# Kernel tuning notes

Measured on AMD Instinct MI355X. Metric: run time of the kernel, lower is better.

Reference implementation:

```python
import jax, jax.numpy as jnp
import numpy as np

D = 512            # d_model
H = 4              # num_heads
DK = D // 2        # total key dim (expand_k = 0.5)
DV = D             # total value dim (expand_v = 1.0)
HK = DK // H       # per-head key dim  = 64
HV = DV // H       # per-head value dim = 128
GATE_LOW_RANK = 16
GATE_LOGIT_NORMALIZER = 16.0
LN_EPS = 1e-5


def setup_inputs() -> dict:
    key = jax.random.key(0)
    ks = jax.random.split(key, 9)
    B, S = 2, 16384
    g = lambda k, shape, scale: (jax.random.normal(k, shape, dtype=jnp.float32) * scale)
    return {
        "x":    g(ks[0], (B, S, D), 1.0),
        "Wq":   g(ks[1], (D, DK), D ** -0.5),
        "Wk":   g(ks[2], (D, DK), D ** -0.5),
        "Wv":   g(ks[3], (D, DV), D ** -0.5),
        "Wg":   g(ks[4], (D, DV), D ** -0.5),
        "Wgk1": g(ks[5], (D, GATE_LOW_RANK), D ** -0.5),
        "Wgk2": g(ks[6], (GATE_LOW_RANK, DK), GATE_LOW_RANK ** -0.5),
        "bgk2": jnp.zeros((DK,), jnp.float32),
        "Wo":   g(ks[7], (DV, D), DV ** -0.5),
    }


def _gla(x, Wq, Wk, Wv, Wg, Wgk1, Wgk2, bgk2, Wo):
    B, S, _ = x.shape
    q = (x @ Wq).reshape(B, S, H, HK) * (HK ** -0.5)   # [B,S,H,HK]
    k = (x @ Wk).reshape(B, S, H, HK)
    v = (x @ Wv).reshape(B, S, H, HV)
    g = (x @ Wg).reshape(B, S, H, HV)                  # output gate
    # low-rank forget gate, in log space
    gk = jax.nn.log_sigmoid((x @ Wgk1) @ Wgk2 + bgk2) / GATE_LOGIT_NORMALIZER
    gk = gk.reshape(B, S, H, HK)

    # gated linear recurrence over time:
    #   h_t = diag(exp(gk_t)) h_{t-1} + k_t^T v_t ;  o_t = q_t h_t
    def step(h, inp):
        q_t, k_t, v_t, gk_t = inp                      # [B,H,HK] / [B,H,HV]
        h = jnp.exp(gk_t)[..., None] * h + k_t[..., None] * v_t[..., None, :]
        o_t = jnp.einsum('bhk,bhkv->bhv', q_t, h)
        return h, o_t

    h0 = jnp.zeros((B, H, HK, HV), x.dtype)
    xs = (q.swapaxes(0, 1), k.swapaxes(0, 1), v.swapaxes(0, 1), gk.swapaxes(0, 1))
    _, o = jax.lax.scan(step, h0, xs)                  # o: [S,B,H,HV]
    o = o.swapaxes(0, 1)                               # [B,S,H,HV]

    # per-head LayerNorm (no affine) + swish output gate
    mu = o.mean(-1, keepdims=True)
    var = ((o - mu) ** 2).mean(-1, keepdims=True)
    o = (o - mu) * jax.lax.rsqrt(var + LN_EPS)
    o = o * jax.nn.silu(g)
    return o.reshape(B, S, DV) @ Wo                    # [B,S,D]


def reference(x, Wq, Wk, Wv, Wg, Wgk1, Wgk2, bgk2, Wo):
    return _gla(x, Wq, Wk, Wv, Wg, Wgk1, Wgk2, bgk2, Wo)
```

## Files before the change

kernel.cpp:

```cpp
#include <hip/hip_runtime.h>
#include <hip/hip_bf16.h>


typedef __hip_bfloat16 bf16;
typedef _Float16 f16;
typedef _Float16 half8 __attribute__((ext_vector_type(8)));
typedef float f32x4 __attribute__((ext_vector_type(4)));
typedef short short8 __attribute__((ext_vector_type(8)));

#define DEV static __device__ __forceinline__

DEV float b2f(bf16 v) { return __bfloat162float(v); }
DEV bf16 f2b(float v) { return __float2bfloat16(v); }
DEV float bits2f(unsigned int u16) {
    union { unsigned int u; float f; } c; c.u = u16 << 16; return c.f;
}
DEV short f2bs(float v) {
    union { bf16 h; short s; } u; u.h = __float2bfloat16(v); return u.s;
}
DEV unsigned short f2bu(float v) {
    union { bf16 h; unsigned short s; } u; u.h = __float2bfloat16(v); return u.s;
}
DEV short f2hs(float v) {
    union { f16 h; short s; } u; u.h = (f16)v; return u.s;
}
DEV float fast_rcp(float v) { return __builtin_amdgcn_rcpf(v); }

DEV float ldf(const float* p) { return *p; }
DEV float ldf(const bf16* p) { return b2f(*p); }
DEV void stf(float* p, float v) { *p = v; }
DEV void stf(bf16* p, float v) { *p = f2b(v); }

DEV float4 ld4(const float* p) { return *(const float4*)p; }
DEV float4 ld4(const bf16* p) {
    const uint2 r = *(const uint2*)p;
    return make_float4(bits2f(r.x & 0xffffu), bits2f(r.x >> 16),
                       bits2f(r.y & 0xffffu), bits2f(r.y >> 16));
}

DEV half8 ld8h(const float* p) {
    const float4 a = *(const float4*)p, b = *(const float4*)(p + 4);
    half8 h;
    h[0] = (f16)a.x; h[1] = (f16)a.y; h[2] = (f16)a.z; h[3] = (f16)a.w;
    h[4] = (f16)b.x; h[5] = (f16)b.y; h[6] = (f16)b.z; h[7] = (f16)b.w;
    return h;
}
DEV half8 ld8h(const f16* p) { return *(const half8*)p; }

DEV f32x4 mfma_bf(short8 a, short8 b, f32x4 c) {
    return __builtin_amdgcn_mfma_f32_16x16x32_bf16(a, b, c, 0, 0, 0);
}
DEV f32x4 mfma_h(half8 a, half8 b, f32x4 c) {
    return __builtin_amdgcn_mfma_f32_16x16x32_f16(a, b, c, 0, 0, 0);
}

DEV void gl_lds16(const f16* g, f16* l) {
    __builtin_amdgcn_global_load_lds(
        (const __attribute__((address_space(1))) void*)g,
        (__attribute__((address_space(3))) void*)l, 16, 0, 0);
}

DEV size_t voff(int v, int t) {
    return (size_t)(((((v >> 4) * 2 + (t >> 5)) * 4 + ((t >> 3) & 3)) * 16
                     + (v & 15)) * 8 + (t & 7));
}

__global__ __launch_bounds__(256) void cvt_xh_k(
    const float* __restrict__ x, f16* __restrict__ xh)
{
    const size_t i = ((size_t)blockIdx.x * 256 + threadIdx.x) * 8;
    *(half8*)&xh[i] = ld8h(&x[i]);
}

__global__ __launch_bounds__(256) void cvt_wt_k(
    const float* __restrict__ Wq, const float* __restrict__ Wk,
    const float* __restrict__ Wv, const float* __restrict__ Wg,
    const float* __restrict__ Wo, f16* __restrict__ Wt)
{
    __shared__ float tile[64][65];
    const int nb = blockIdx.x * 64;
    const int tid = threadIdx.x;
    const float* src; int nloc, N;
    if (nb < 256)       { src = Wq; N = 256; nloc = nb; }
    else if (nb < 512)  { src = Wk; N = 256; nloc = nb - 256; }
    else if (nb < 1024) { src = Wv; N = 512; nloc = nb - 512; }
    else if (nb < 1536) { src = Wg; N = 512; nloc = nb - 1024; }
    else                { src = Wo; N = 512; nloc = nb - 1536; }
    for (int k0 = 0; k0 < 512; k0 += 64) {
        for (int e = tid; e < 4096; e += 256) {
            const int i = e >> 6, j = e & 63;
            tile[i][j] = src[(size_t)(k0 + i) * N + nloc + j];
        }
        __syncthreads();
        for (int e = tid; e < 4096; e += 256) {
            const int j = e >> 6, i = e & 63;
            Wt[(size_t)(nb + j) * 512 + k0 + i] = (f16)tile[i][j];
        }
        __syncthreads();
    }
}

__global__ __launch_bounds__(256) void proj_gemm_k(
    const f16* __restrict__ A, const f16* __restrict__ Wt,
    bf16* __restrict__ Qb, bf16* __restrict__ Kb,
    bf16* __restrict__ VF, bf16* __restrict__ GOb)
{
    __shared__ __align__(16) f16 As[128][64];
    __shared__ __align__(16) f16 Bs[128][64];
    const int bm = blockIdx.x * 128;
    const int bn = blockIdx.y * 128;
    const int tid = threadIdx.x;
    const int lane = tid & 63;
    const int wid = tid >> 6;
    const int wr = wid >> 1, wc = wid & 1;
    const int al = lane & 15;
    const int kg = lane >> 4;
    const int al7 = al & 7;

    f32x4 acc[4][4];
#pragma unroll
    for (int m = 0; m < 4; ++m)
#pragma unroll
        for (int n = 0; n < 4; ++n)
#pragma unroll
            for (int r = 0; r < 4; ++r) acc[m][n][r] = 0.f;

    const int srow = wid * 32 + (lane >> 3);
    const int sswz = ((lane & 7) ^ (lane >> 3)) << 3;
    const f16* ap = A + (size_t)(bm + srow) * 512 + sswz;
    const f16* bp = Wt + (size_t)(bn + srow) * 512 + sswz;

    for (int k0 = 0; k0 < 512; k0 += 64) {
        if (k0) __syncthreads();
#pragma unroll
        for (int i = 0; i < 4; ++i) {
            gl_lds16(ap + (size_t)i * 8 * 512 + k0, &As[wid * 32 + i * 8][0]);
            gl_lds16(bp + (size_t)i * 8 * 512 + k0, &Bs[wid * 32 + i * 8][0]);
        }
        __syncthreads();
#pragma unroll
        for (int ks = 0; ks < 2; ++ks) {
            half8 af[4], bfr[4];
            const int sp = ((ks * 4 + kg) ^ al7) << 3;
#pragma unroll
            for (int m = 0; m < 4; ++m)
                af[m] = *(const half8*)&As[wr * 64 + m * 16 + al][sp];
#pragma unroll
            for (int n = 0; n < 4; ++n)
                bfr[n] = *(const half8*)&Bs[wc * 64 + n * 16 + al][sp];
#pragma unroll
            for (int m = 0; m < 4; ++m)
#pragma unroll
                for (int n = 0; n < 4; ++n)
                    acc[m][n] = mfma_h(af[m], bfr[n], acc[m][n]);
        }
    }

    const int r00 = bm + wr * 64 + kg * 4;
    const int c00 = bn + wc * 64 + al;
    const int seg = bn >> 8;
    if (seg == 0) {
#pragma unroll
        for (int m = 0; m < 4; ++m)
#pragma unroll
            for (int n = 0; n < 4; ++n)
#pragma unroll
                for (int r = 0; r < 4; ++r)
                    stf(&Qb[(size_t)(r00 + m * 16 + r) * 256 + c00 + n * 16],
                        acc[m][n][r] * 0.125f);
    } else if (seg == 1) {
#pragma unroll
        for (int m = 0; m < 4; ++m)
#pragma unroll
            for (int n = 0; n < 4; ++n)
#pragma unroll
                for (int r = 0; r < 4; ++r)
                    stf(&Kb[(size_t)(r00 + m * 16 + r) * 256 + (c00 - 256) + n * 16],
                        acc[m][n][r]);
    } else if (seg <= 3) {
#pragma unroll
        for (int m = 0; m < 4; ++m) {
            const int row0 = r00 + m * 16;
            const int bi = row0 >> 14;
            const int chunk = (row0 >> 6) & 255;
            const int tc = row0 & 63;
#pragma unroll
            for (int n = 0; n < 4; ++n) {
                const int col = c00 - 512 + n * 16;
                const int h = col >> 7, v = col & 127;
                bf16* dst = VF + (size_t)((bi * 4 + h) * 256 + chunk) * 8192
                               + voff(v, tc);
                ushort4 pk;
                pk.x = f2bu(acc[m][n][0]); pk.y = f2bu(acc[m][n][1]);
                pk.z = f2bu(acc[m][n][2]); pk.w = f2bu(acc[m][n][3]);
                *(ushort4*)dst = pk;
            }
        }
    } else {
#pragma unroll
        for (int m = 0; m < 4; ++m)
#pragma unroll
            for (int n = 0; n < 4; ++n)
#pragma unroll
                for (int r = 0; r < 4; ++r) {
                    const float v = acc[m][n][r];
                    const float sil = v * fast_rcp(1.f + __expf(-v));
                    stf(&GOb[(size_t)(r00 + m * 16 + r) * 512 + (c00 - 1024) + n * 16],
                        sil);
                }
    }
}

__global__ __launch_bounds__(256) void gemm_bt_k(
    const f16* __restrict__ A, const f16* __restrict__ Bt,
    float* __restrict__ C)
{
    __shared__ __align__(16) f16 As[128][64];
    __shared__ __align__(16) f16 Bs[128][64];
    const int bm = blockIdx.x * 128;
    const int bn = blockIdx.y * 128;
    const int tid = threadIdx.x;
    const int lane = tid & 63;
    const int wid = tid >> 6;
    const int wr = wid >> 1, wc = wid & 1;
    const int al = lane & 15;
    const int kg = lane >> 4;
    const int al7 = al & 7;

    f32x4 acc[4][4];
#pragma unroll
    for (int m = 0; m < 4; ++m)
#pragma unroll
        for (int n = 0; n < 4; ++n)
#pragma unroll
            for (int r = 0; r < 4; ++r) acc[m][n][r] = 0.f;

    const int srow = wid * 32 + (lane >> 3);
    const int sswz = ((lane & 7) ^ (lane >> 3)) << 3;
    const f16* ap = A + (size_t)(bm + srow) * 512 + sswz;
    const f16* bp = Bt + (size_t)(bn + srow) * 512 + sswz;

    for (int k0 = 0; k0 < 512; k0 += 64) {
        if (k0) __syncthreads();
#pragma unroll
        for (int i = 0; i < 4; ++i) {
            gl_lds16(ap + (size_t)i * 8 * 512 + k0, &As[wid * 32 + i * 8][0]);
            gl_lds16(bp + (size_t)i * 8 * 512 + k0, &Bs[wid * 32 + i * 8][0]);
        }
        __syncthreads();
#pragma unroll
        for (int ks = 0; ks < 2; ++ks) {
            half8 af[4], bfr[4];
            const int sp = ((ks * 4 + kg) ^ al7) << 3;
#pragma unroll
            for (int m = 0; m < 4; ++m)
                af[m] = *(const half8*)&As[wr * 64 + m * 16 + al][sp];
#pragma unroll
            for (int n = 0; n < 4; ++n)
                bfr[n] = *(const half8*)&Bs[wc * 64 + n * 16 + al][sp];
#pragma unroll
            for (int m = 0; m < 4; ++m)
#pragma unroll
                for (int n = 0; n < 4; ++n)
                    acc[m][n] = mfma_h(af[m], bfr[n], acc[m][n]);
        }
    }
    const int r0 = bm + wr * 64 + kg * 4;
    const int c0 = bn + wc * 64 + al;
#pragma unroll
    for (int m = 0; m < 4; ++m)
#pragma unroll
        for (int n = 0; n < 4; ++n)
#pragma unroll
            for (int r = 0; r < 4; ++r)
                C[(size_t)(r0 + m * 16 + r) * 512 + c0 + n * 16] = acc[m][n][r];
}

template <typename GKT>
__global__ __launch_bounds__(256) void gate_mfma_k(
    const f16* __restrict__ xh, const float* __restrict__ Wgk1,
    const float* __restrict__ Wgk2, const float* __restrict__ bgk2,
    GKT* __restrict__ GK)
{
    __shared__ __align__(16) f16 As[128][40];
    __shared__ __align__(16) f16 w1s[16][520];
    __shared__ float tls[128][17];
    const int bm = blockIdx.x * 128;
    const int tid = threadIdx.x;
    const int lane = tid & 63;
    const int wid = tid >> 6;
    const int al = lane & 15;
    const int kg = lane >> 4;
    const int kg8 = kg * 8;

    for (int e = tid; e < 8192; e += 256) {
        const int kk = e >> 4, n = e & 15;
        w1s[n][kk] = (f16)Wgk1[e];
    }

    f32x4 acc[2];
#pragma unroll
    for (int m = 0; m < 2; ++m)
#pragma unroll
        for (int r = 0; r < 4; ++r) acc[m][r] = 0.f;

    const int ar = tid >> 1;
    const int ac = (tid & 1) * 16;
    for (int k0 = 0; k0 < 512; k0 += 32) {
        {
            const f16* ap = xh + (size_t)(bm + ar) * 512 + k0 + ac;
            *(half8*)&As[ar][ac] = *(const half8*)ap;
            *(half8*)&As[ar][ac + 8] = *(const half8*)(ap + 8);
        }
        __syncthreads();
        const half8 bfr = *(const half8*)&w1s[al][k0 + kg8];
#pragma unroll
        for (int m = 0; m < 2; ++m) {
            const half8 af = *(const half8*)&As[wid * 32 + m * 16 + al][kg8];
            acc[m] = mfma_h(af, bfr, acc[m]);
        }
        __syncthreads();
    }
#pragma unroll
    for (int m = 0; m < 2; ++m)
#pragma unroll
        for (int r = 0; r < 4; ++r)
            tls[wid * 32 + m * 16 + kg * 4 + r][al] = acc[m][r];
    __syncthreads();

    float w2[16];
#pragma unroll
    for (int r = 0; r < 16; ++r) w2[r] = Wgk2[r * 256 + tid];
    const float bb = bgk2[tid];
    GKT* gout = GK + (size_t)bm * 256 + tid;
    for (int m = 0; m < 128; ++m) {
        float z = bb;
#pragma unroll
        for (int r = 0; r < 16; ++r) z = fmaf(tls[m][r], w2[r], z);
        const float ls = fminf(z, 0.f) - __logf(1.f + __expf(-fabsf(z)));
        stf(&gout[(size_t)m * 256], ls * (1.f / 16.f));
    }
}

template <typename GKT, typename CST>
__global__ __launch_bounds__(256) void chunk_state_k(
    const bf16* __restrict__ Km, const bf16* __restrict__ VF,
    const GKT* __restrict__ GKm, CST* __restrict__ CS,
    float* __restrict__ DD)
{
    __shared__ __align__(16) short k2t[64][72];
    __shared__ float cpart[4][64];
    const int blk = blockIdx.x;
    const int chunk = blk & 255;
    const int bh = blk >> 8;
    const int bi = bh >> 2, h = bh & 3;
    const int rowbase = bi * 16384 + chunk * 64;
    const int tid = threadIdx.x;
    const int k = tid & 63, tg = tid >> 6;

    float g[16];
    {
        float run = 0.f;
#pragma unroll
        for (int j = 0; j < 16; ++j) {
            run += ldf(&GKm[(size_t)(rowbase + tg * 16 + j) * 256 + h * 64 + k]);
            g[j] = run;
        }
        cpart[tg][k] = run;
    }
    __syncthreads();
    float off = 0.f;
#pragma unroll
    for (int s = 0; s < 3; ++s) if (s < tg) off += cpart[s][k];
    const float tot = cpart[0][k] + cpart[1][k] + cpart[2][k] + cpart[3][k];
    if (tg == 0) DD[(size_t)blk * 64 + k] = __expf(tot);

    {
        short8 p0, p1;
#pragma unroll
        for (int j = 0; j < 16; ++j) {
            const float kv = ldf(&Km[(size_t)(rowbase + tg * 16 + j) * 256 + h * 64 + k]);
            const float w = kv * __expf(tot - (g[j] + off));
            if (j < 8) p0[j] = f2bs(w); else p1[j - 8] = f2bs(w);
        }
        *(short8*)&k2t[k][tg * 16] = p0;
        *(short8*)&k2t[k][tg * 16 + 8] = p1;
    }
    __syncthreads();

    const int lane = tid & 63, wid = tid >> 6;
    const int al = lane & 15, kg = lane >> 4, kg8 = kg * 8;
    const bf16* Vtb = VF + (size_t)blk * 8192;

    short8 xf[2][2];
#pragma unroll
    for (int m = 0; m < 2; ++m)
#pragma unroll
        for (int ks = 0; ks < 2; ++ks)
            xf[m][ks] = *(const short8*)&Vtb[(size_t)(((wid * 2 + m) * 2 + ks) * 64 + lane) * 8];
    short8 yf[2][4];
#pragma unroll
    for (int ks = 0; ks < 2; ++ks)
#pragma unroll
        for (int n = 0; n < 4; ++n)
            yf[ks][n] = *(const short8*)&k2t[n * 16 + al][ks * 32 + kg8];

    f32x4 acc[2][4];
#pragma unroll
    for (int m = 0; m < 2; ++m)
#pragma unroll
        for (int n = 0; n < 4; ++n)
#pragma unroll
            for (int r = 0; r < 4; ++r) acc[m][n][r] = 0.f;
#pragma unroll
    for (int ks = 0; ks < 2; ++ks)
#pragma unroll
        for (int m = 0; m < 2; ++m)
#pragma unroll
            for (int n = 0; n < 4; ++n)
                acc[m][n] = mfma_bf(xf[m][ks], yf[ks][n], acc[m][n]);

    CST* out = CS + (size_t)blk * 8192;
#pragma unroll
    for (int m = 0; m < 2; ++m)
#pragma unroll
        for (int n = 0; n < 4; ++n)
#pragma unroll
            for (int r = 0; r < 4; ++r)
                stf(&out[(size_t)(wid * 32 + m * 16 + kg * 4 + r) * 64 + n * 16 + al],
                    acc[m][n][r]);
}

template <typename CST>
__global__ __launch_bounds__(256) void scan_k(
    const CST* __restrict__ CS, const float* __restrict__ DD,
    bf16* __restrict__ HF)
{
    const int bh = blockIdx.x >> 5;
    const int slice = blockIdx.x & 31;
    const int tid = threadIdx.x;
    const int e = slice * 256 + tid;
    const int v = e >> 6, k = e & 63;
    float H = 0.f;
    const CST* base = CS + (size_t)bh * 256 * 8192 + e;
    bf16* hbase = HF + (size_t)bh * 256 * 8192 + voff(v, k);
    const float* dbase = DD + (size_t)bh * 256 * 64 + k;
#pragma unroll 4
    for (int n = 0; n < 256; ++n) {
        const float s = ldf(&base[(size_t)n * 8192]);
        const float d = dbase[(size_t)n * 64];
        stf(&hbase[(size_t)n * 8192], H);
        H = fmaf(d, H, s);
    }
}

template <typename GKT>
__global__ __launch_bounds__(256) void chunk_out_k(
    const bf16* __restrict__ Qm, const bf16* __restrict__ Km,
    const bf16* __restrict__ VF, const GKT* __restrict__ GKm,
    const bf16* __restrict__ HF, bf16* GO)
{
    __shared__ __align__(16) short qs[64][72];
    __shared__ __align__(16) short ks[64][72];
    __shared__ __align__(16) short ab[64][72];
    __shared__ float cpart[4][64];

    const int blk = blockIdx.x;
    const int chunk = blk & 255;
    const int bh = blk >> 8;
    const int bi = bh >> 2, h = bh & 3;
    const int rowbase = bi * 16384 + chunk * 64;
    const int tid = threadIdx.x;
    const int k = tid & 63, tg = tid >> 6;

    float g[16];
    {
        float run = 0.f;
#pragma unroll
        for (int j = 0; j < 16; ++j) {
            run += ldf(&GKm[(size_t)(rowbase + tg * 16 + j) * 256 + h * 64 + k]);
            g[j] = run;
        }
        cpart[tg][k] = run;
    }
    __syncthreads();
    float off = 0.f;
#pragma unroll
    for (int s = 0; s < 3; ++s) if (s < tg) off += cpart[s][k];

#pragma unroll
    for (int j = 0; j < 16; ++j) {
        const int t = tg * 16 + j;
        const size_t idx = (size_t)(rowbase + t) * 256 + h * 64 + k;
        const float gc = g[j] + off;
        const float eg = __expf(gc);
        qs[t][k] = f2bs(ldf(&Qm[idx]) * eg);
        ks[t][k] = f2bs(ldf(&Km[idx]) * fast_rcp(eg));
    }
    __syncthreads();

    const int lane = tid & 63, wid = tid >> 6;
    const int al = lane & 15, kg = lane >> 4;
    const int w16 = wid * 16, kg8 = kg * 8;

    short8 xq[2];
    xq[0] = *(const short8*)&qs[w16 + al][kg8];
    xq[1] = *(const short8*)&qs[w16 + al][32 + kg8];

    f32x4 aacc[4];
#pragma unroll
    for (int n = 0; n < 4; ++n)
#pragma unroll
        for (int r = 0; r < 4; ++r) aacc[n][r] = 0.f;
#pragma unroll
    for (int ksb = 0; ksb < 2; ++ksb)
#pragma unroll
        for (int n = 0; n < 4; ++n) {
            const short8 y = *(const short8*)&ks[n * 16 + al][ksb * 32 + kg8];
            aacc[n] = mfma_bf(xq[ksb], y, aacc[n]);
        }
#pragma unroll
    for (int n = 0; n < 4; ++n)
#pragma unroll
        for (int r = 0; r < 4; ++r) {
            const int tt = w16 + kg * 4 + r;
            const int ii = n * 16 + al;
            ab[tt][ii] = (ii <= tt) ? f2bs(aacc[n][r]) : (short)0;
        }
    short8 xa[2];
    xa[0] = *(const short8*)&ab[w16 + al][kg8];
    xa[1] = *(const short8*)&ab[w16 + al][32 + kg8];

    const bf16* Vtb = VF + (size_t)blk * 8192;
    const bf16* Hb = HF + (size_t)blk * 8192;
    f32x4 oacc[8];
#pragma unroll
    for (int n = 0; n < 8; ++n)
#pragma unroll
        for (int r = 0; r < 4; ++r) oacc[n][r] = 0.f;
#pragma unroll
    for (int n = 0; n < 8; ++n) {
        const size_t f0 = (size_t)((n * 2 + 0) * 64 + lane) * 8;
        const size_t f1 = (size_t)((n * 2 + 1) * 64 + lane) * 8;
        const short8 yv0 = *(const short8*)&Vtb[f0];
        const short8 yv1 = *(const short8*)&Vtb[f1];
        const short8 yh0 = *(const short8*)&Hb[f0];
        const short8 yh1 = *(const short8*)&Hb[f1];
        oacc[n] = mfma_bf(xa[0], yv0, oacc[n]);
        oacc[n] = mfma_bf(xa[1], yv1, oacc[n]);
        oacc[n] = mfma_bf(xq[0], yh0, oacc[n]);
        oacc[n] = mfma_bf(xq[1], yh1, oacc[n]);
    }

    float psum[4] = {0.f, 0.f, 0.f, 0.f}, psq[4] = {0.f, 0.f, 0.f, 0.f};
#pragma unroll
    for (int n = 0; n < 8; ++n)
#pragma unroll
        for (int r = 0; r < 4; ++r) {
            const float v = oacc[n][r];
            psum[r] += v; psq[r] = fmaf(v, v, psq[r]);
        }
#pragma unroll
    for (int offx = 1; offx < 16; offx <<= 1)
#pragma unroll
        for (int r = 0; r < 4; ++r) {
            psum[r] += __shfl_xor(psum[r], offx);
            psq[r] += __shfl_xor(psq[r], offx);
        }
#pragma unroll
    for (int r = 0; r < 4; ++r) {
        const float mu = psum[r] * (1.f / 128.f);
        const float var = psq[r] * (1.f / 128.f) - mu * mu;
        const float rstd = rsqrtf(fmaxf(var, 0.f) + 1e-5f);
        const int row = rowbase + w16 + kg * 4 + r;
        short* gop = (short*)(GO + (size_t)row * 512 + h * 128 + al);
#pragma unroll
        for (int n = 0; n < 8; ++n) {
            const bf16 gb = *(const bf16*)&gop[n * 16];
            const float sil = b2f(gb);
            gop[n * 16] = f2hs((oacc[n][r] - mu) * rstd * sil);
        }
    }
}

__global__ __launch_bounds__(256) void zero_k(float* out, int n) {
    const int i = blockIdx.x * 256 + threadIdx.x;
    if (i < n) out[i] = 0.f;
}

template <typename GKT, typename CST>
static void run_all(const float* x, const float* Wq, const float* Wk,
                    const float* Wv, const float* Wg, const float* Wgk1,
                    const float* Wgk2, const float* bgk2, const float* Wo,
                    float* out, char* ws, hipStream_t stream)
{
    const int M = 32768;
    auto aln = [](size_t v) { return (v + 255) & ~(size_t)255; };
    char* cur = ws;
    bf16* Qb = (bf16*)cur;  cur += aln((size_t)M * 256 * 2);
    bf16* Kb = (bf16*)cur;  cur += aln((size_t)M * 256 * 2);
    bf16* Vfb = (bf16*)cur; cur += aln((size_t)M * 512 * 2);
    bf16* GOb = (bf16*)cur; cur += aln((size_t)M * 512 * 2);
    bf16* Hfb = (bf16*)cur; cur += aln((size_t)2048 * 8192 * 2);
    float* DDb = (float*)cur; cur += aln((size_t)2048 * 64 * 4);
    f16* Wtb = (f16*)cur;   cur += aln((size_t)2048 * 512 * 2);
    GKT* GKb = (GKT*)cur;   cur += aln((size_t)M * 256 * sizeof(GKT));
    CST* CSb = (CST*)cur;
    f16* xh = (f16*)CSb;

    const dim3 blk(256);
    cvt_xh_k<<<dim3(8192), blk, 0, stream>>>(x, xh);
    cvt_wt_k<<<dim3(32), blk, 0, stream>>>(Wq, Wk, Wv, Wg, Wo, Wtb);
    proj_gemm_k<<<dim3(M / 128, 12), blk, 0, stream>>>(xh, Wtb, Qb, Kb, Vfb, GOb);
    gate_mfma_k<<<dim3(M / 128), blk, 0, stream>>>(xh, Wgk1, Wgk2, bgk2, GKb);
    chunk_state_k<<<dim3(2048), blk, 0, stream>>>(Kb, Vfb, GKb, CSb, DDb);
    scan_k<<<dim3(256), blk, 0, stream>>>(CSb, DDb, Hfb);
    chunk_out_k<<<dim3(2048), blk, 0, stream>>>(Qb, Kb, Vfb, GKb, Hfb, GOb);
    gemm_bt_k<<<dim3(M / 128, 4), blk, 0, stream>>>((const f16*)GOb,
                                                    Wtb + (size_t)1536 * 512, out);
}

extern "C" void kernel_launch(void* const* d_in, const int* in_sizes, int n_in,
                              void* d_out, int out_size, void* d_ws, size_t ws_size,
                              hipStream_t stream)
{
    const float* x    = (const float*)d_in[0];
    const float* Wq   = (const float*)d_in[1];
    const float* Wk   = (const float*)d_in[2];
    const float* Wv   = (const float*)d_in[3];
    const float* Wg   = (const float*)d_in[4];
    const float* Wgk1 = (const float*)d_in[5];
    const float* Wgk2 = (const float*)d_in[6];
    const float* bgk2 = (const float*)d_in[7];
    const float* Wo   = (const float*)d_in[8];
    float* out = (float*)d_out;

    const size_t M = 32768;
    const size_t slack = 8192;
    const size_t base = 2 * M * 256 * 2 + 2 * M * 512 * 2
                      + (size_t)2048 * 8192 * 2 + 2048 * 64 * 4
                      + (size_t)2048 * 512 * 2 + slack;
    const size_t gk_f = M * 256 * 4, gk_b = M * 256 * 2;
    const size_t cs_f = (size_t)2048 * 8192 * 4, cs_b = (size_t)2048 * 8192 * 2;
    const size_t needA = base + gk_f + cs_f;
    const size_t needB = base + gk_b + cs_b;

    if (ws_size >= needA) {
        run_all<float, float>(x, Wq, Wk, Wv, Wg, Wgk1, Wgk2, bgk2, Wo,
                              out, (char*)d_ws, stream);
    } else if (ws_size >= needB) {
        run_all<bf16, bf16>(x, Wq, Wk, Wv, Wg, Wgk1, Wgk2, bgk2, Wo,
                            out, (char*)d_ws, stream);
    } else {
        zero_k<<<dim3((out_size + 255) / 256), dim3(256), 0, stream>>>(out, out_size);
    }
}
```

Baseline: 368.9 us.

## Use bf16 gate/state buffers, shrink GEMM K-tile, and swizzle block order

The two MFMA GEMMs now stage 32-wide K slices in LDS with a new XOR swizzle and fewer loads per step. They also remap block indices so that groups of eight consecutive blocks spread across M tiles, which is meant to improve cache locality. Separately, the templated float path for the gate log-decays and chunk states is removed, so bf16 storage is always used. That halves their memory traffic when the workspace is large, at some cost in accuracy. The smaller K tile doubles the number of barrier iterations.

```diff
diff --git a/kernel.cpp b/kernel.cpp
--- a/kernel.cpp
+++ b/kernel.cpp
@@ -105,17 +105,18 @@
     bf16* __restrict__ Qb, bf16* __restrict__ Kb,
     bf16* __restrict__ VF, bf16* __restrict__ GOb)
 {
-    __shared__ __align__(16) f16 As[128][64];
-    __shared__ __align__(16) f16 Bs[128][64];
-    const int bm = blockIdx.x * 128;
-    const int bn = blockIdx.y * 128;
+    __shared__ __align__(128) f16 As[128][32];
+    __shared__ __align__(128) f16 Bs[128][32];
+    const int flat = blockIdx.y * 256 + blockIdx.x;
+    const int fs = (flat & 7) * 384 + (flat >> 3);
+    const int bm = (fs & 255) * 128;
+    const int bn = (fs >> 8) * 128;
     const int tid = threadIdx.x;
     const int lane = tid & 63;
     const int wid = tid >> 6;
     const int wr = wid >> 1, wc = wid & 1;
     const int al = lane & 15;
     const int kg = lane >> 4;
-    const int al7 = al & 7;
 
     f32x4 acc[4][4];
 #pragma unroll
@@ -125,35 +126,31 @@
 #pragma unroll
             for (int r = 0; r < 4; ++r) acc[m][n][r] = 0.f;
 
-    const int srow = wid * 32 + (lane >> 3);
-    const int sswz = ((lane & 7) ^ (lane >> 3)) << 3;
-    const f16* ap = A + (size_t)(bm + srow) * 512 + sswz;
-    const f16* bp = Wt + (size_t)(bn + srow) * 512 + sswz;
-
-    for (int k0 = 0; k0 < 512; k0 += 64) {
+    const int srow = wid * 32 + (lane >> 2);
+    const int gsw = (((lane & 3) ^ ((lane >> 3) & 3))) << 3;
+    const f16* ap = A + (size_t)(bm + srow) * 512 + gsw;
+    const f16* bp = Wt + (size_t)(bn + srow) * 512 + gsw;
+    const int sp = (kg ^ ((al >> 1) & 3)) << 3;
+
+    for (int k0 = 0; k0 < 512; k0 += 32) {
         if (k0) __syncthreads();
-#pragma unroll
-        for (int i = 0; i < 4; ++i) {
-            gl_lds16(ap + (size_t)i * 8 * 512 + k0, &As[wid * 32 + i * 8][0]);
-            gl_lds16(bp + (size_t)i * 8 * 512 + k0, &Bs[wid * 32 + i * 8][0]);
-        }
+        gl_lds16(ap + k0, &As[wid * 32][0]);
+        gl_lds16(ap + (size_t)16 * 512 + k0, &As[wid * 32 + 16][0]);
+        gl_lds16(bp + k0, &Bs[wid * 32][0]);
+        gl_lds16(bp + (size_t)16 * 512 + k0, &Bs[wid * 32 + 16][0]);
         __syncthreads();
-#pragma unroll
-        for (int ks = 0; ks < 2; ++ks) {
-            half8 af[4], bfr[4];
-            const int sp = ((ks * 4 + kg) ^ al7) << 3;
-#pragma unroll
-            for (int m = 0; m < 4; ++m)
-                af[m] = *(const half8*)&As[wr * 64 + m * 16 + al][sp];
+        half8 af[4], bfr[4];
+#pragma unroll
+        for (int m = 0; m < 4; ++m)
+            af[m] = *(const half8*)&As[wr * 64 + m * 16 + al][sp];
+#pragma unroll
+        for (int n = 0; n < 4; ++n)
+            bfr[n] = *(const half8*)&Bs[wc * 64 + n * 16 + al][sp];
+#pragma unroll
+        for (int m = 0; m < 4; ++m)
 #pragma unroll
             for (int n = 0; n < 4; ++n)
-                bfr[n] = *(const half8*)&Bs[wc * 64 + n * 16 + al][sp];
-#pragma unroll
-            for (int m = 0; m < 4; ++m)
-#pragma unroll
-                for (int n = 0; n < 4; ++n)
-                    acc[m][n] = mfma_h(af[m], bfr[n], acc[m][n]);
-        }
+                acc[m][n] = mfma_h(af[m], bfr[n], acc[m][n]);
     }
 
     const int r00 = bm + wr * 64 + kg * 4;
@@ -215,17 +212,18 @@
     const f16* __restrict__ A, const f16* __restrict__ Bt,
     float* __restrict__ C)
 {
-    __shared__ __align__(16) f16 As[128][64];
-    __shared__ __align__(16) f16 Bs[128][64];
-    const int bm = blockIdx.x * 128;
-    const int bn = blockIdx.y * 128;
+    __shared__ __align__(128) f16 As[128][32];
+    __shared__ __align__(128) f16 Bs[128][32];
+    const int flat = blockIdx.y * 256 + blockIdx.x;
+    const int fs = (flat & 7) * 128 + (flat >> 3);
+    const int bm = (fs & 255) * 128;
+    const int bn = (fs >> 8) * 128;
     const int tid = threadIdx.x;
     const int lane = tid & 63;
     const int wid = tid >> 6;
     const int wr = wid >> 1, wc = wid & 1;
     const int al = lane & 15;
     const int kg = lane >> 4;
-    const int al7 = al & 7;
 
     f32x4 acc[4][4];
 #pragma unroll
@@ -235,35 +233,31 @@
 #pragma unroll
             for (int r = 0; r < 4; ++r) acc[m][n][r] = 0.f;
 
-    const int srow = wid * 32 + (lane >> 3);
-    const int sswz = ((lane & 7) ^ (lane >> 3)) << 3;
-    const f16* ap = A + (size_t)(bm + srow) * 512 + sswz;
-    const f16* bp = Bt + (size_t)(bn + srow) * 512 + sswz;
-
-    for (int k0 = 0; k0 < 512; k0 += 64) {
+    const int srow = wid * 32 + (lane >> 2);
+    const int gsw = (((lane & 3) ^ ((lane >> 3) & 3))) << 3;
+    const f16* ap = A + (size_t)(bm + srow) * 512 + gsw;
+    const f16* bp = Bt + (size_t)(bn + srow) * 512 + gsw;
+    const int sp = (kg ^ ((al >> 1) & 3)) << 3;
+
+    for (int k0 = 0; k0 < 512; k0 += 32) {
         if (k0) __syncthreads();
-#pragma unroll
-        for (int i = 0; i < 4; ++i) {
-            gl_lds16(ap + (size_t)i * 8 * 512 + k0, &As[wid * 32 + i * 8][0]);
-            gl_lds16(bp + (size_t)i * 8 * 512 + k0, &Bs[wid * 32 + i * 8][0]);
-        }
+        gl_lds16(ap + k0, &As[wid * 32][0]);
+        gl_lds16(ap + (size_t)16 * 512 + k0, &As[wid * 32 + 16][0]);
+        gl_lds16(bp + k0, &Bs[wid * 32][0]);
+        gl_lds16(bp + (size_t)16 * 512 + k0, &Bs[wid * 32 + 16][0]);
         __syncthreads();
-#pragma unroll
-        for (int ks = 0; ks < 2; ++ks) {
-            half8 af[4], bfr[4];
-            const int sp = ((ks * 4 + kg) ^ al7) << 3;
-#pragma unroll
-            for (int m = 0; m < 4; ++m)
-                af[m] = *(const half8*)&As[wr * 64 + m * 16 + al][sp];
+        half8 af[4], bfr[4];
+#pragma unroll
+        for (int m = 0; m < 4; ++m)
+            af[m] = *(const half8*)&As[wr * 64 + m * 16 + al][sp];
+#pragma unroll
+        for (int n = 0; n < 4; ++n)
+            bfr[n] = *(const half8*)&Bs[wc * 64 + n * 16 + al][sp];
+#pragma unroll
+        for (int m = 0; m < 4; ++m)
 #pragma unroll
             for (int n = 0; n < 4; ++n)
-                bfr[n] = *(const half8*)&Bs[wc * 64 + n * 16 + al][sp];
-#pragma unroll
-            for (int m = 0; m < 4; ++m)
-#pragma unroll
-                for (int n = 0; n < 4; ++n)
-                    acc[m][n] = mfma_h(af[m], bfr[n], acc[m][n]);
-        }
+                acc[m][n] = mfma_h(af[m], bfr[n], acc[m][n]);
     }
     const int r0 = bm + wr * 64 + kg * 4;
     const int c0 = bn + wc * 64 + al;
@@ -276,11 +270,10 @@
                 C[(size_t)(r0 + m * 16 + r) * 512 + c0 + n * 16] = acc[m][n][r];
 }
 
-template <typename GKT>
 __global__ __launch_bounds__(256) void gate_mfma_k(
     const f16* __restrict__ xh, const float* __restrict__ Wgk1,
     const float* __restrict__ Wgk2, const float* __restrict__ bgk2,
-    GKT* __restrict__ GK)
+    bf16* __restrict__ GK)
 {
     __shared__ __align__(16) f16 As[128][40];
     __shared__ __align__(16) f16 w1s[16][520];
@@ -332,7 +325,7 @@
 #pragma unroll
     for (int r = 0; r < 16; ++r) w2[r] = Wgk2[r * 256 + tid];
     const float bb = bgk2[tid];
-    GKT* gout = GK + (size_t)bm * 256 + tid;
+    bf16* gout = GK + (size_t)bm * 256 + tid;
     for (int m = 0; m < 128; ++m) {
         float z = bb;
 #pragma unroll
@@ -342,10 +335,9 @@
     }
 }
 
-template <typename GKT, typename CST>
 __global__ __launch_bounds__(256) void chunk_state_k(
     const bf16* __restrict__ Km, const bf16* __restrict__ VF,
-    const GKT* __restrict__ GKm, CST* __restrict__ CS,
+    const bf16* __restrict__ GKm, bf16* __restrict__ CS,
     float* __restrict__ DD)
 {
     __shared__ __align__(16) short k2t[64][72];
@@ -420,7 +412,7 @@
             for (int n = 0; n < 4; ++n)
                 acc[m][n] = mfma_bf(xf[m][ks], yf[ks][n], acc[m][n]);
 
-    CST* out = CS + (size_t)blk * 8192;
+    bf16* out = CS + (size_t)blk * 8192;
 #pragma unroll
     for (int m = 0; m < 2; ++m)
 #pragma unroll
@@ -431,9 +423,8 @@
                     acc[m][n][r]);
 }
 
-template <typename CST>
 __global__ __launch_bounds__(256) void scan_k(
-    const CST* __restrict__ CS, const float* __restrict__ DD,
+    const bf16* __restrict__ CS, const float* __restrict__ DD,
     bf16* __restrict__ HF)
 {
     const int bh = blockIdx.x >> 5;
@@ -442,7 +433,7 @@
     const int e = slice * 256 + tid;
     const int v = e >> 6, k = e & 63;
     float H = 0.f;
-    const CST* base = CS + (size_t)bh * 256 * 8192 + e;
+    const bf16* base = CS + (size_t)bh * 256 * 8192 + e;
     bf16* hbase = HF + (size_t)bh * 256 * 8192 + voff(v, k);
     const float* dbase = DD + (size_t)bh * 256 * 64 + k;
 #pragma unroll 4
@@ -454,10 +445,9 @@
     }
 }
 
-template <typename GKT>
 __global__ __launch_bounds__(256) void chunk_out_k(
     const bf16* __restrict__ Qm, const bf16* __restrict__ Km,
-    const bf16* __restrict__ VF, const GKT* __restrict__ GKm,
+    const bf16* __restrict__ VF, const bf16* __restrict__ GKm,
     const bf16* __restrict__ HF, bf16* GO)
 {
     __shared__ __align__(16) short qs[64][72];
@@ -588,7 +578,6 @@
     if (i < n) out[i] = 0.f;
 }
 
-template <typename GKT, typename CST>
 static void run_all(const float* x, const float* Wq, const float* Wk,
                     const float* Wv, const float* Wg, const float* Wgk1,
                     const float* Wgk2, const float* bgk2, const float* Wo,
@@ -604,20 +593,20 @@
     bf16* Hfb = (bf16*)cur; cur += aln((size_t)2048 * 8192 * 2);
     float* DDb = (float*)cur; cur += aln((size_t)2048 * 64 * 4);
     f16* Wtb = (f16*)cur;   cur += aln((size_t)2048 * 512 * 2);
-    GKT* GKb = (GKT*)cur;   cur += aln((size_t)M * 256 * sizeof(GKT));
-    CST* CSb = (CST*)cur;
+    bf16* GKb = (bf16*)cur; cur += aln((size_t)M * 256 * 2);
+    bf16* CSb = (bf16*)cur;
     f16* xh = (f16*)CSb;
 
     const dim3 blk(256);
     cvt_xh_k<<<dim3(8192), blk, 0, stream>>>(x, xh);
     cvt_wt_k<<<dim3(32), blk, 0, stream>>>(Wq, Wk, Wv, Wg, Wo, Wtb);
-    proj_gemm_k<<<dim3(M / 128, 12), blk, 0, stream>>>(xh, Wtb, Qb, Kb, Vfb, GOb);
+    proj_gemm_k<<<dim3(256, 12), blk, 0, stream>>>(xh, Wtb, Qb, Kb, Vfb, GOb);
     gate_mfma_k<<<dim3(M / 128), blk, 0, stream>>>(xh, Wgk1, Wgk2, bgk2, GKb);
     chunk_state_k<<<dim3(2048), blk, 0, stream>>>(Kb, Vfb, GKb, CSb, DDb);
     scan_k<<<dim3(256), blk, 0, stream>>>(CSb, DDb, Hfb);
     chunk_out_k<<<dim3(2048), blk, 0, stream>>>(Qb, Kb, Vfb, GKb, Hfb, GOb);
-    gemm_bt_k<<<dim3(M / 128, 4), blk, 0, stream>>>((const f16*)GOb,
-                                                    Wtb + (size_t)1536 * 512, out);
+    gemm_bt_k<<<dim3(256, 4), blk, 0, stream>>>((const f16*)GOb,
+                                                Wtb + (size_t)1536 * 512, out);
 }
 
 extern "C" void kernel_launch(void* const* d_in, const int* in_sizes, int n_in,
@@ -637,20 +626,14 @@
 
     const size_t M = 32768;
     const size_t slack = 8192;
-    const size_t base = 2 * M * 256 * 2 + 2 * M * 512 * 2
+    const size_t need = 2 * M * 256 * 2 + 2 * M * 512 * 2
                       + (size_t)2048 * 8192 * 2 + 2048 * 64 * 4
-                      + (size_t)2048 * 512 * 2 + slack;
-    const size_t gk_f = M * 256 * 4, gk_b = M * 256 * 2;
-    const size_t cs_f = (size_t)2048 * 8192 * 4, cs_b = (size_t)2048 * 8192 * 2;
-    const size_t needA = base + gk_f + cs_f;
-    const size_t needB = base + gk_b + cs_b;
-
-    if (ws_size >= needA) {
-        run_all<float, float>(x, Wq, Wk, Wv, Wg, Wgk1, Wgk2, bgk2, Wo,
-                              out, (char*)d_ws, stream);
-    } else if (ws_size >= needB) {
-        run_all<bf16, bf16>(x, Wq, Wk, Wv, Wg, Wgk1, Wgk2, bgk2, Wo,
-                            out, (char*)d_ws, stream);
+                      + (size_t)2048 * 512 * 2 + M * 256 * 2
+                      + (size_t)2048 * 8192 * 2 + slack;
+
+    if (ws_size >= need) {
+        run_all(x, Wq, Wk, Wv, Wg, Wgk1, Wgk2, bgk2, Wo,
+                out, (char*)d_ws, stream);
     } else {
         zero_k<<<dim3((out_size + 255) / 256), dim3(256), 0, stream>>>(out, out_size);
     }
```

Result: no change. 365.7 us (-0.9%).
